# Kernel optimization log

Measured on AMD Instinct MI355X. Metric: run time of the kernel, lower is better.

## Reference

```python
import jax, jax.numpy as jnp
import numpy as np

N_HEAD = 16
MASKED_BIAS = -10000.0


def setup_inputs() -> dict:
    key = jax.random.key(0)
    k1, k2, k3 = jax.random.split(key, 3)
    B, S, D = 2, 2048, 1024
    scale_in = 0.02  # GPT-2 style init scale for weights
    return {
        "hidden_states": jax.random.normal(k1, (B, S, D), dtype=jnp.float32),
        "c_attn_w": jax.random.normal(k2, (D, 3 * D), dtype=jnp.float32) * scale_in,
        "c_attn_b": jnp.zeros((3 * D,), dtype=jnp.float32),
        "c_proj_w": jax.random.normal(k3, (D, D), dtype=jnp.float32) * scale_in,
        "c_proj_b": jnp.zeros((D,), dtype=jnp.float32),
    }


def reference(hidden_states, c_attn_w, c_attn_b, c_proj_w, c_proj_b):
    B, S, D = hidden_states.shape
    H = N_HEAD
    hd = D // H

    # Conv1D (HF): x @ W + b, fused QKV
    qkv = hidden_states @ c_attn_w + c_attn_b          # [B, S, 3D]
    q, k, v = jnp.split(qkv, 3, axis=-1)

    def to_heads(x):  # [B, S, D] -> [B, H, S, hd]
        return x.reshape(B, S, H, hd).transpose(0, 2, 1, 3)

    q, k, v = to_heads(q), to_heads(k), to_heads(v)

    # scaled scores (scale=True divides by sqrt(head_dim))
    w = jnp.einsum("bhqd,bhkd->bhqk", q, k) / jnp.float32(hd) ** 0.5  # [B,H,S,S]

    # causal mask via torch.where(mask, w, masked_bias)
    causal = jnp.tril(jnp.ones((S, S), dtype=bool))
    w = jnp.where(causal, w, jnp.float32(MASKED_BIAS))

    w = jax.nn.softmax(w, axis=-1)
    # attn_dropout / resid_dropout are identity in eval mode

    out = jnp.einsum("bhqk,bhkd->bhqd", w, v)          # [B,H,S,hd]
    out = out.transpose(0, 2, 1, 3).reshape(B, S, D)   # merge heads

    return out @ c_proj_w + c_proj_b                   # [B,S,D]
```

## Files before the change

kernel.cpp:

```cpp
#include <hip/hip_runtime.h>
#include <hip/hip_bf16.h>

typedef __attribute__((ext_vector_type(8))) short bf16x8;
typedef __attribute__((ext_vector_type(4))) float f32x4;
typedef __attribute__((ext_vector_type(4))) unsigned u32x4;

#define B_SZ 2
#define S_SZ 2048
#define D_SZ 1024
#define H_SZ 16
#define HD_SZ 64

static __device__ __forceinline__ short f2bf(float f) {
    unsigned u = __builtin_bit_cast(unsigned, f);
    u += 0x7FFFu + ((u >> 16) & 1u);
    return (short)(u >> 16);
}

static __device__ __forceinline__ float fexp2(float x) {
    float r; asm("v_exp_f32 %0, %1" : "=v"(r) : "v"(x)); return r;
}

static __device__ __forceinline__ unsigned cvtpk(float lo, float hi) {
    unsigned r; asm("v_cvt_pk_bf16_f32 %0, %1, %2" : "=v"(r) : "v"(lo), "v"(hi)); return r;
}

static __device__ __forceinline__ void gload16(const short* g, short* l) {
    __builtin_amdgcn_global_load_lds(
        (const __attribute__((address_space(1))) unsigned*)g,
        (__attribute__((address_space(3))) unsigned*)l,
        16, 0, 0);
}

#define SBAR() do { __builtin_amdgcn_sched_barrier(0); \
                    __builtin_amdgcn_s_barrier(); \
                    __builtin_amdgcn_sched_barrier(0); } while (0)

__global__ __launch_bounds__(256) void k_prep(const float* __restrict__ hs, short* __restrict__ Xb,
                                              const float* __restrict__ w1, short* __restrict__ W1T,
                                              const float* __restrict__ w2, short* __restrict__ W2T) {
    __shared__ float tile[32][33];
    const int id = blockIdx.x;
    const int tid = threadIdx.x;
    if (id < 4096) {
        int i = (id * 256 + tid) * 4;
        float4 v = *reinterpret_cast<const float4*>(hs + i);
        short4 o;
        o.x = f2bf(v.x); o.y = f2bf(v.y); o.z = f2bf(v.z); o.w = f2bf(v.w);
        *reinterpret_cast<short4*>(Xb + i) = o;
        return;
    }
    const float* in;
    short* out;
    int N, bx, by;
    if (id < 7168) {
        int bid = id - 4096;
        in = w1; out = W1T; N = 3072;
        bx = bid % 96; by = bid / 96;
    } else {
        int bid = id - 7168;
        in = w2; out = W2T; N = 1024;
        bx = bid & 31; by = bid >> 5;
    }
    const int k0 = by * 32, n0 = bx * 32;
    const int tx = tid & 31, ty = tid >> 5;
    #pragma unroll
    for (int i = 0; i < 4; ++i)
        tile[ty + i * 8][tx] = in[(size_t)(k0 + ty + i * 8) * N + n0 + tx];
    __syncthreads();
    #pragma unroll
    for (int i = 0; i < 4; ++i)
        out[(size_t)(n0 + ty + i * 8) * 1024 + k0 + tx] = f2bf(tile[tx][ty + i * 8]);
}

__global__ __launch_bounds__(512, 1) void k_gemm_qkv8(
    const short* __restrict__ A, const short* __restrict__ Bt,
    const float* __restrict__ bias,
    short* __restrict__ Qo, short* __restrict__ Ko, short* __restrict__ VTo) {
    constexpr int K = 1024, NT = 16;
    __shared__ short As[2][256 * 64];
    __shared__ short Bs[2][192 * 64];
    const int tid = threadIdx.x;
    const int lane = tid & 63;
    const int w = tid >> 6;
    const int wr = w >> 2, wc = w & 3;
    const int lr = lane & 15, lc = lane >> 4;
    const int bid = blockIdx.x;
    const int xcd = bid & 7, local = bid >> 3;
    const int bm = (xcd >> 1) * 4 + (local >> 3);
    const int bn = (xcd & 1) * 8 + (local & 7);
    const size_t arow0 = (size_t)bm * 256;
    const size_t brow0 = (size_t)bn * 192;

    const int srl = tid >> 3;
    const int sc8 = (tid & 7) ^ (srl & 7);
    const int dcol = (tid & 7) * 8;

    f32x4 acc[8][3];
    #pragma unroll
    for (int m = 0; m < 8; ++m)
        #pragma unroll
        for (int n = 0; n < 3; ++n)
            acc[m][n] = (f32x4){0.f, 0.f, 0.f, 0.f};

    auto STAGE_A = [&](int T) {
        const int buf = T & 1;
        #pragma unroll
        for (int j = 0; j < 4; ++j) {
            int row = j * 64 + srl;
            gload16(&A[(arow0 + row) * K + T * 64 + sc8 * 8], &As[buf][row * 64 + dcol]);
        }
    };
    auto STAGE_B = [&](int T) {
        const int buf = T & 1;
        #pragma unroll
        for (int j = 0; j < 3; ++j) {
            int row = j * 64 + srl;
            gload16(&Bt[(brow0 + row) * K + T * 64 + sc8 * 8], &Bs[buf][row * 64 + dcol]);
        }
    };

    const int rx = (lr & 7) * 8;
    auto LDA = [&](int buf, int rowoff, int c) {
        return *reinterpret_cast<const bf16x8*>(
            &As[buf][(wr * 128 + rowoff + lr) * 64 + (((c * 32) + lc * 8) ^ rx)]);
    };
    auto LDB = [&](int buf, int n, int c) {
        return *reinterpret_cast<const bf16x8*>(
            &Bs[buf][(wc * 48 + n * 16 + lr) * 64 + (((c * 32) + lc * 8) ^ rx)]);
    };

    bf16x8 at[4][2];
    bf16x8 bfr[3][2];

    STAGE_A(0); STAGE_B(0); STAGE_B(1);
    asm volatile("s_waitcnt vmcnt(3)" ::: "memory");
    SBAR();

    for (int T = 0; T < NT; ++T) {
        const int buf = T & 1;
        #pragma unroll
        for (int m = 0; m < 4; ++m)
            #pragma unroll
            for (int c = 0; c < 2; ++c)
                at[m][c] = LDA(buf, m * 16, c);
        #pragma unroll
        for (int n = 0; n < 3; ++n)
            #pragma unroll
            for (int c = 0; c < 2; ++c)
                bfr[n][c] = LDB(buf, n, c);
        if (T + 1 < NT) STAGE_A(T + 1);
        SBAR();
        __builtin_amdgcn_s_setprio(1);
        #pragma unroll
        for (int m = 0; m < 4; ++m)
            #pragma unroll
            for (int n = 0; n < 3; ++n)
                #pragma unroll
                for (int c = 0; c < 2; ++c)
                    acc[m][n] = __builtin_amdgcn_mfma_f32_16x16x32_bf16(at[m][c], bfr[n][c], acc[m][n], 0, 0, 0);
        __builtin_amdgcn_s_setprio(0);
        SBAR();
        #pragma unroll
        for (int m = 0; m < 4; ++m)
            #pragma unroll
            for (int c = 0; c < 2; ++c)
                at[m][c] = LDA(buf, 64 + m * 16, c);
        if (T + 2 < NT) {
            STAGE_B(T + 2);
            asm volatile("s_waitcnt vmcnt(3)" ::: "memory");
        } else {
            asm volatile("s_waitcnt vmcnt(0)" ::: "memory");
        }
        SBAR();
        __builtin_amdgcn_s_setprio(1);
        #pragma unroll
        for (int m = 0; m < 4; ++m)
            #pragma unroll
            for (int n = 0; n < 3; ++n)
                #pragma unroll
                for (int c = 0; c < 2; ++c)
                    acc[4 + m][n] = __builtin_amdgcn_mfma_f32_16x16x32_bf16(at[m][c], bfr[n][c], acc[4 + m][n], 0, 0, 0);
        __builtin_amdgcn_s_setprio(0);
        SBAR();
    }

    #pragma unroll
    for (int n = 0; n < 3; ++n) {
        const int col = bn * 192 + wc * 48 + n * 16 + lr;
        const float bv = bias[col];
        if (col < 2048) {
            const bool isq = (col < 1024);
            const float scale = isq ? 0.18033688011112042f : 1.0f;
            short* dst = isq ? Qo : Ko;
            const int dg = col & 1023;
            const int hh = dg >> 6, dd = dg & 63;
            #pragma unroll
            for (int m = 0; m < 8; ++m) {
                #pragma unroll
                for (int r = 0; r < 4; ++r) {
                    int grow = bm * 256 + wr * 128 + m * 16 + lc * 4 + r;
                    int b = grow >> 11, s = grow & 2047;
                    dst[(((size_t)(b * H_SZ + hh)) * S_SZ + s) * HD_SZ + dd] = f2bf((acc[m][n][r] + bv) * scale);
                }
            }
        } else {
            const int dv = col - 2048;
            const int hh = dv >> 6, dt = dv & 63;
            #pragma unroll
            for (int m = 0; m < 8; ++m) {
                int grow = bm * 256 + wr * 128 + m * 16 + lc * 4;
                int b = grow >> 11, s = grow & 2047;
                short4 st;
                st.x = f2bf(acc[m][n][0] + bv);
                st.y = f2bf(acc[m][n][1] + bv);
                st.z = f2bf(acc[m][n][2] + bv);
                st.w = f2bf(acc[m][n][3] + bv);
                *reinterpret_cast<short4*>(
                    &VTo[(((size_t)(b * H_SZ + hh)) * HD_SZ + dt) * S_SZ + s]) = st;
            }
        }
    }
}

__global__ __launch_bounds__(256) void k_attn(const short* __restrict__ Q,
                                              const short* __restrict__ Kv,
                                              const short* __restrict__ VT,
                                              short* __restrict__ O) {
    __shared__ short Ks[3][64 * 64];
    __shared__ short Vs[3][64 * 64];
    const int id = blockIdx.x;
    const int bh = ((id & 7) << 2) | ((id >> 3) & 3);
    const int h = bh & 15;
    const int bb = bh >> 4;
    const int g = id >> 5, oct = g >> 3, gr = g & 7;
    const int qt = (oct == 0) ? 31 - gr : (oct == 1) ? 16 + gr : (oct == 2) ? 15 - gr : gr;
    const int tid = threadIdx.x;
    const int lane = tid & 63, w = tid >> 6;
    const int lr = lane & 15, lc = lane >> 4;
    const int qrow0 = qt * 64 + w * 16;
    const size_t base = (size_t)bh * S_SZ * HD_SZ;

    bf16x8 qf[2];
    #pragma unroll
    for (int c = 0; c < 2; ++c)
        qf[c] = *reinterpret_cast<const bf16x8*>(&Q[base + (size_t)(qrow0 + lr) * HD_SZ + c * 32 + lc * 8]);

    float l_run = 0.f;
    f32x4 o_acc[4];
    #pragma unroll
    for (int n = 0; n < 4; ++n) o_acc[n] = (f32x4){0.f, 0.f, 0.f, 0.f};

    const int srow = tid >> 3;
    const int sslot = (tid & 7) ^ (srow & 7);
    const short* kp = &Kv[base + (size_t)srow * HD_SZ + sslot * 8];
    const short* vp = &VT[base + (size_t)srow * S_SZ + sslot * 8];
    auto STAGE = [&](int b) {
        gload16(kp, &Ks[b][tid * 8]);
        gload16(kp + 2048, &Ks[b][2048 + tid * 8]);
        gload16(vp, &Vs[b][tid * 8]);
        gload16(vp + 32 * S_SZ, &Vs[b][2048 + tid * 8]);
        kp += 4096; vp += 64;
    };

    const int q_row = qrow0 + lr;
    const int rxa = (lr & 7) * 8;
    const bool b0 = (lane & 16) != 0;
    const bool b1 = (lane & 32) != 0;

    STAGE(0);
    if (qt >= 1) {
        STAGE(1);
        asm volatile("s_waitcnt vmcnt(4)" ::: "memory");
    } else {
        asm volatile("s_waitcnt vmcnt(0)" ::: "memory");
    }
    SBAR();

    int bufc = 0, stc = 2;
    for (int kt = 0; kt <= qt; ++kt) {
        if (kt + 2 <= qt) STAGE(stc);
        {
            f32x4 sf[4];
            __builtin_amdgcn_s_setprio(1);
            #pragma unroll
            for (int n = 0; n < 4; ++n) {
                f32x4 z = (f32x4){0.f, 0.f, 0.f, 0.f};
                #pragma unroll
                for (int c = 0; c < 2; ++c) {
                    bf16x8 kf = *reinterpret_cast<const bf16x8*>(
                        &Ks[bufc][(n * 16 + lr) * 64 + ((c * 32 + lc * 8) ^ rxa)]);
                    z = __builtin_amdgcn_mfma_f32_16x16x32_bf16(kf, qf[c], z, 0, 0, 0);
                }
                sf[n] = z;
            }
            __builtin_amdgcn_s_setprio(0);
            if (kt == qt) {
                const int kb = kt * 64 + lc * 4 - q_row;
                #pragma unroll
                for (int n = 0; n < 4; ++n)
                    #pragma unroll
                    for (int r = 0; r < 4; ++r)
                        sf[n][r] = (kb + n * 16 + r > 0) ? -14427.0f : sf[n][r];
            }
            float rs = 0.f;
            #pragma unroll
            for (int n = 0; n < 4; ++n)
                #pragma unroll
                for (int r = 0; r < 4; ++r) {
                    float pv = fexp2(sf[n][r]);
                    sf[n][r] = pv;
                    rs += pv;
                }
            l_run += rs;
            unsigned Apk0 = cvtpk(sf[0][0], sf[0][1]), Apk1 = cvtpk(sf[0][2], sf[0][3]);
            unsigned Bpk0 = cvtpk(sf[1][0], sf[1][1]), Bpk1 = cvtpk(sf[1][2], sf[1][3]);
            unsigned Cpk0 = cvtpk(sf[2][0], sf[2][1]), Cpk1 = cvtpk(sf[2][2], sf[2][3]);
            unsigned Dpk0 = cvtpk(sf[3][0], sf[3][1]), Dpk1 = cvtpk(sf[3][2], sf[3][3]);
            unsigned x0 = __shfl_xor(b0 ? Apk0 : Bpk0, 16);
            unsigned x1 = __shfl_xor(b0 ? Apk1 : Bpk1, 16);
            unsigned x2 = __shfl_xor(b0 ? Cpk0 : Dpk0, 16);
            unsigned x3 = __shfl_xor(b0 ? Cpk1 : Dpk1, 16);
            unsigned y0 = __shfl_xor(b1 ? Apk0 : Bpk0, 32);
            unsigned y1 = __shfl_xor(b1 ? Apk1 : Bpk1, 32);
            unsigned y2 = __shfl_xor(b1 ? Cpk0 : Dpk0, 32);
            unsigned y3 = __shfl_xor(b1 ? Cpk1 : Dpk1, 32);
            unsigned z0 = __shfl_xor(b1 ? Apk0 : Bpk0, 48);
            unsigned z1 = __shfl_xor(b1 ? Apk1 : Bpk1, 48);
            unsigned z2 = __shfl_xor(b1 ? Cpk0 : Dpk0, 48);
            unsigned z3 = __shfl_xor(b1 ? Cpk1 : Dpk1, 48);
            u32x4 pv0 = { b1 ? (b0 ? x0 : y0) : (b0 ? z0 : Apk0),
                          b1 ? (b0 ? x1 : y1) : (b0 ? z1 : Apk1),
                          b1 ? (b0 ? Bpk0 : z0) : (b0 ? y0 : x0),
                          b1 ? (b0 ? Bpk1 : z1) : (b0 ? y1 : x1) };
            u32x4 pv1 = { b1 ? (b0 ? x2 : y2) : (b0 ? z2 : Cpk0),
                          b1 ? (b0 ? x3 : y3) : (b0 ? z3 : Cpk1),
                          b1 ? (b0 ? Dpk0 : z2) : (b0 ? y2 : x2),
                          b1 ? (b0 ? Dpk1 : z3) : (b0 ? y3 : x3) };
            bf16x8 paA = __builtin_bit_cast(bf16x8, pv0);
            bf16x8 paB = __builtin_bit_cast(bf16x8, pv1);
            __builtin_amdgcn_s_setprio(1);
            #pragma unroll
            for (int c = 0; c < 2; ++c) {
                bf16x8 pa = c ? paB : paA;
                #pragma unroll
                for (int n = 0; n < 4; ++n) {
                    bf16x8 vf = *reinterpret_cast<const bf16x8*>(
                        &Vs[bufc][(n * 16 + lr) * 64 + ((c * 32 + lc * 8) ^ rxa)]);
                    o_acc[n] = __builtin_amdgcn_mfma_f32_16x16x32_bf16(pa, vf, o_acc[n], 0, 0, 0);
                }
            }
            __builtin_amdgcn_s_setprio(0);
        }
        if (kt < qt) {
            if (kt + 2 <= qt) asm volatile("s_waitcnt vmcnt(4)" ::: "memory");
            else              asm volatile("s_waitcnt vmcnt(0)" ::: "memory");
            SBAR();
        }
        bufc = (bufc == 2) ? 0 : bufc + 1;
        stc  = (stc == 2) ? 0 : stc + 1;
    }

    l_run += __shfl_xor(l_run, 16);
    l_run += __shfl_xor(l_run, 32);
    float li[4];
    #pragma unroll
    for (int r = 0; r < 4; ++r)
        li[r] = 1.0f / __shfl(l_run, lc * 4 + r);
    #pragma unroll
    for (int n = 0; n < 4; ++n) {
        #pragma unroll
        for (int r = 0; r < 4; ++r) {
            float v = o_acc[n][r] * li[r];
            int s = qrow0 + lc * 4 + r;
            O[((size_t)bb * S_SZ + s) * D_SZ + h * 64 + n * 16 + lr] = f2bf(v);
        }
    }
}

__global__ __launch_bounds__(256, 2) void k_gemm_proj(
    const short* __restrict__ A, const short* __restrict__ Bt,
    const float* __restrict__ bias, float* __restrict__ out) {
    constexpr int K = 1024, NT = 16, N = 1024;
    __shared__ short As[2][128 * 64];
    __shared__ short Bs[2][128 * 64];
    const int tid = threadIdx.x;
    const int lane = tid & 63;
    const int w = tid >> 6;
    const int wr = w >> 1, wc = w & 1;
    const int lr = lane & 15, lc = lane >> 4;
    const int bid = blockIdx.x;
    const int xcd = bid & 7, local = bid >> 3;
    const int bm = xcd * 4 + (local & 3);
    const int bn = local >> 2;
    const size_t arow0 = (size_t)bm * 128;
    const size_t brow0 = (size_t)bn * 128;

    const int srl = tid >> 3;
    const int sc8 = (tid & 7) ^ (srl & 7);
    const int dcol = (tid & 7) * 8;

    f32x4 acc[4][4];
    #pragma unroll
    for (int m = 0; m < 4; ++m)
        #pragma unroll
        for (int n = 0; n < 4; ++n)
            acc[m][n] = (f32x4){0.f, 0.f, 0.f, 0.f};

    auto STAGE_A = [&](int T) {
        const int buf = T & 1;
        #pragma unroll
        for (int j = 0; j < 4; ++j) {
            int row = j * 32 + srl;
            gload16(&A[(arow0 + row) * K + T * 64 + sc8 * 8], &As[buf][row * 64 + dcol]);
        }
    };
    auto STAGE_B = [&](int T) {
        const int buf = T & 1;
        #pragma unroll
        for (int j = 0; j < 4; ++j) {
            int row = j * 32 + srl;
            gload16(&Bt[(brow0 + row) * K + T * 64 + sc8 * 8], &Bs[buf][row * 64 + dcol]);
        }
    };

    const int rx = (lr & 7) * 8;
    auto LDA = [&](int buf, int rowoff, int c) {
        return *reinterpret_cast<const bf16x8*>(
            &As[buf][(wr * 64 + rowoff + lr) * 64 + (((c * 32) + lc * 8) ^ rx)]);
    };
    auto LDB = [&](int buf, int n, int c) {
        return *reinterpret_cast<const bf16x8*>(
            &Bs[buf][(wc * 64 + n * 16 + lr) * 64 + (((c * 32) + lc * 8) ^ rx)]);
    };

    bf16x8 at[2][2];
    bf16x8 bfr[4][2];

    STAGE_A(0); STAGE_B(0); STAGE_B(1);
    asm volatile("s_waitcnt vmcnt(4)" ::: "memory");
    SBAR();

    for (int T = 0; T < NT; ++T) {
        const int buf = T & 1;
        #pragma unroll
        for (int m = 0; m < 2; ++m)
            #pragma unroll
            for (int c = 0; c < 2; ++c)
                at[m][c] = LDA(buf, m * 16, c);
        #pragma unroll
        for (int n = 0; n < 4; ++n)
            #pragma unroll
            for (int c = 0; c < 2; ++c)
                bfr[n][c] = LDB(buf, n, c);
        if (T + 1 < NT) STAGE_A(T + 1);
        SBAR();
        __builtin_amdgcn_s_setprio(1);
        #pragma unroll
        for (int m = 0; m < 2; ++m)
            #pragma unroll
            for (int n = 0; n < 4; ++n)
                #pragma unroll
                for (int c = 0; c < 2; ++c)
                    acc[m][n] = __builtin_amdgcn_mfma_f32_16x16x32_bf16(at[m][c], bfr[n][c], acc[m][n], 0, 0, 0);
        __builtin_amdgcn_s_setprio(0);
        SBAR();
        #pragma unroll
        for (int m = 0; m < 2; ++m)
            #pragma unroll
            for (int c = 0; c < 2; ++c)
                at[m][c] = LDA(buf, 32 + m * 16, c);
        if (T + 2 < NT) {
            STAGE_B(T + 2);
            asm volatile("s_waitcnt vmcnt(4)" ::: "memory");
        } else {
            asm volatile("s_waitcnt vmcnt(0)" ::: "memory");
        }
        SBAR();
        __builtin_amdgcn_s_setprio(1);
        #pragma unroll
        for (int m = 0; m < 2; ++m)
            #pragma unroll
            for (int n = 0; n < 4; ++n)
                #pragma unroll
                for (int c = 0; c < 2; ++c)
                    acc[2 + m][n] = __builtin_amdgcn_mfma_f32_16x16x32_bf16(at[m][c], bfr[n][c], acc[2 + m][n], 0, 0, 0);
        __builtin_amdgcn_s_setprio(0);
        SBAR();
    }

    #pragma unroll
    for (int n = 0; n < 4; ++n) {
        const int col = bn * 128 + wc * 64 + n * 16 + lr;
        const float bv = bias[col];
        #pragma unroll
        for (int m = 0; m < 4; ++m) {
            #pragma unroll
            for (int r = 0; r < 4; ++r) {
                int grow = bm * 128 + wr * 64 + m * 16 + lc * 4 + r;
                out[(size_t)grow * N + col] = acc[m][n][r] + bv;
            }
        }
    }
}

extern "C" void kernel_launch(void* const* d_in, const int* in_sizes, int n_in,
                              void* d_out, int out_size, void* d_ws, size_t ws_size,
                              hipStream_t stream) {
    (void)in_sizes; (void)n_in; (void)out_size; (void)ws_size;
    const float* hs     = (const float*)d_in[0];
    const float* w_attn = (const float*)d_in[1];
    const float* b_attn = (const float*)d_in[2];
    const float* w_proj = (const float*)d_in[3];
    const float* b_proj = (const float*)d_in[4];
    float* out = (float*)d_out;
    char* ws = (char*)d_ws;

    short* Xb  = (short*)(ws + 0);
    short* W1T = (short*)(ws + 8388608);
    short* W2T = (short*)(ws + 14680064);
    short* Qb  = (short*)(ws + 16777216);
    short* Kb  = (short*)(ws + 25165824);
    short* VTb = (short*)(ws + 33554432);
    short* Ob  = (short*)(ws + 0);

    k_prep<<<dim3(8192), dim3(256), 0, stream>>>(hs, Xb, w_attn, W1T, w_proj, W2T);
    k_gemm_qkv8<<<dim3(256), dim3(512), 0, stream>>>(Xb, W1T, b_attn, Qb, Kb, VTb);
    k_attn<<<dim3(1024), dim3(256), 0, stream>>>(Qb, Kb, VTb, Ob);
    k_gemm_proj<<<dim3(256), dim3(256), 0, stream>>>(Ob, W2T, b_proj, out);
}
```

Before: 98.12 us.

## Software-pipeline QK^T of next tile with softmax and PV of current tile

```diff
diff --git a/kernel.cpp b/kernel.cpp
--- a/kernel.cpp
+++ b/kernel.cpp
@@ -227,8 +227,8 @@
                                               const short* __restrict__ Kv,
                                               const short* __restrict__ VT,
                                               short* __restrict__ O) {
-    __shared__ short Ks[3][64 * 64];
-    __shared__ short Vs[3][64 * 64];
+    __shared__ short Ks[4][64 * 64];
+    __shared__ short Vs[4][64 * 64];
     const int id = blockIdx.x;
     const int bh = ((id & 7) << 2) | ((id >> 3) & 3);
     const int h = bh & 15;
@@ -268,6 +268,22 @@
     const bool b0 = (lane & 16) != 0;
     const bool b1 = (lane & 32) != 0;
 
+    auto QK = [&](f32x4* s, int b) {
+        __builtin_amdgcn_s_setprio(1);
+        #pragma unroll
+        for (int n = 0; n < 4; ++n) {
+            f32x4 z = (f32x4){0.f, 0.f, 0.f, 0.f};
+            #pragma unroll
+            for (int c = 0; c < 2; ++c) {
+                bf16x8 kf = *reinterpret_cast<const bf16x8*>(
+                    &Ks[b][(n * 16 + lr) * 64 + ((c * 32 + lc * 8) ^ rxa)]);
+                z = __builtin_amdgcn_mfma_f32_16x16x32_bf16(kf, qf[c], z, 0, 0, 0);
+            }
+            s[n] = z;
+        }
+        __builtin_amdgcn_s_setprio(0);
+    };
+
     STAGE(0);
     if (qt >= 1) {
         STAGE(1);
@@ -276,89 +292,78 @@
         asm volatile("s_waitcnt vmcnt(0)" ::: "memory");
     }
     SBAR();
-
-    int bufc = 0, stc = 2;
-    for (int kt = 0; kt <= qt; ++kt) {
-        if (kt + 2 <= qt) STAGE(stc);
-        {
-            f32x4 sf[4];
-            __builtin_amdgcn_s_setprio(1);
-            #pragma unroll
-            for (int n = 0; n < 4; ++n) {
-                f32x4 z = (f32x4){0.f, 0.f, 0.f, 0.f};
-                #pragma unroll
-                for (int c = 0; c < 2; ++c) {
-                    bf16x8 kf = *reinterpret_cast<const bf16x8*>(
-                        &Ks[bufc][(n * 16 + lr) * 64 + ((c * 32 + lc * 8) ^ rxa)]);
-                    z = __builtin_amdgcn_mfma_f32_16x16x32_bf16(kf, qf[c], z, 0, 0, 0);
-                }
-                sf[n] = z;
-            }
-            __builtin_amdgcn_s_setprio(0);
-            if (kt == qt) {
-                const int kb = kt * 64 + lc * 4 - q_row;
-                #pragma unroll
-                for (int n = 0; n < 4; ++n)
-                    #pragma unroll
-                    for (int r = 0; r < 4; ++r)
-                        sf[n][r] = (kb + n * 16 + r > 0) ? -14427.0f : sf[n][r];
-            }
-            float rs = 0.f;
+    f32x4 sf[4];
+    QK(sf, 0);
+
+    for (int i = 0; i <= qt; ++i) {
+        const int bcur = i & 3, bnext = (i + 1) & 3, bst = (i + 2) & 3;
+        if (i + 2 <= qt) {
+            STAGE(bst);
+            asm volatile("s_waitcnt vmcnt(4)" ::: "memory");
+        } else {
+            asm volatile("s_waitcnt vmcnt(0)" ::: "memory");
+        }
+        SBAR();
+        f32x4 sfn[4];
+        if (i < qt) QK(sfn, bnext);
+        if (i == qt) {
+            const int kb = i * 64 + lc * 4 - q_row;
             #pragma unroll
             for (int n = 0; n < 4; ++n)
                 #pragma unroll
-                for (int r = 0; r < 4; ++r) {
-                    float pv = fexp2(sf[n][r]);
-                    sf[n][r] = pv;
-                    rs += pv;
-                }
-            l_run += rs;
-            unsigned Apk0 = cvtpk(sf[0][0], sf[0][1]), Apk1 = cvtpk(sf[0][2], sf[0][3]);
-            unsigned Bpk0 = cvtpk(sf[1][0], sf[1][1]), Bpk1 = cvtpk(sf[1][2], sf[1][3]);
-            unsigned Cpk0 = cvtpk(sf[2][0], sf[2][1]), Cpk1 = cvtpk(sf[2][2], sf[2][3]);
-            unsigned Dpk0 = cvtpk(sf[3][0], sf[3][1]), Dpk1 = cvtpk(sf[3][2], sf[3][3]);
-            unsigned x0 = __shfl_xor(b0 ? Apk0 : Bpk0, 16);
-            unsigned x1 = __shfl_xor(b0 ? Apk1 : Bpk1, 16);
-            unsigned x2 = __shfl_xor(b0 ? Cpk0 : Dpk0, 16);
-            unsigned x3 = __shfl_xor(b0 ? Cpk1 : Dpk1, 16);
-            unsigned y0 = __shfl_xor(b1 ? Apk0 : Bpk0, 32);
-            unsigned y1 = __shfl_xor(b1 ? Apk1 : Bpk1, 32);
-            unsigned y2 = __shfl_xor(b1 ? Cpk0 : Dpk0, 32);
-            unsigned y3 = __shfl_xor(b1 ? Cpk1 : Dpk1, 32);
-            unsigned z0 = __shfl_xor(b1 ? Apk0 : Bpk0, 48);
-            unsigned z1 = __shfl_xor(b1 ? Apk1 : Bpk1, 48);
-            unsigned z2 = __shfl_xor(b1 ? Cpk0 : Dpk0, 48);
-            unsigned z3 = __shfl_xor(b1 ? Cpk1 : Dpk1, 48);
-            u32x4 pv0 = { b1 ? (b0 ? x0 : y0) : (b0 ? z0 : Apk0),
-                          b1 ? (b0 ? x1 : y1) : (b0 ? z1 : Apk1),
-                          b1 ? (b0 ? Bpk0 : z0) : (b0 ? y0 : x0),
-                          b1 ? (b0 ? Bpk1 : z1) : (b0 ? y1 : x1) };
-            u32x4 pv1 = { b1 ? (b0 ? x2 : y2) : (b0 ? z2 : Cpk0),
-                          b1 ? (b0 ? x3 : y3) : (b0 ? z3 : Cpk1),
-                          b1 ? (b0 ? Dpk0 : z2) : (b0 ? y2 : x2),
-                          b1 ? (b0 ? Dpk1 : z3) : (b0 ? y3 : x3) };
-            bf16x8 paA = __builtin_bit_cast(bf16x8, pv0);
-            bf16x8 paB = __builtin_bit_cast(bf16x8, pv1);
-            __builtin_amdgcn_s_setprio(1);
-            #pragma unroll
-            for (int c = 0; c < 2; ++c) {
-                bf16x8 pa = c ? paB : paA;
-                #pragma unroll
-                for (int n = 0; n < 4; ++n) {
-                    bf16x8 vf = *reinterpret_cast<const bf16x8*>(
-                        &Vs[bufc][(n * 16 + lr) * 64 + ((c * 32 + lc * 8) ^ rxa)]);
-                    o_acc[n] = __builtin_amdgcn_mfma_f32_16x16x32_bf16(pa, vf, o_acc[n], 0, 0, 0);
-                }
+                for (int r = 0; r < 4; ++r)
+                    sf[n][r] = (kb + n * 16 + r > 0) ? -14427.0f : sf[n][r];
+        }
+        float rs = 0.f;
+        #pragma unroll
+        for (int n = 0; n < 4; ++n)
+            #pragma unroll
+            for (int r = 0; r < 4; ++r) {
+                float pv = fexp2(sf[n][r]);
+                sf[n][r] = pv;
+                rs += pv;
             }
-            __builtin_amdgcn_s_setprio(0);
-        }
-        if (kt < qt) {
-            if (kt + 2 <= qt) asm volatile("s_waitcnt vmcnt(4)" ::: "memory");
-            else              asm volatile("s_waitcnt vmcnt(0)" ::: "memory");
-            SBAR();
-        }
-        bufc = (bufc == 2) ? 0 : bufc + 1;
-        stc  = (stc == 2) ? 0 : stc + 1;
+        l_run += rs;
+        unsigned Apk0 = cvtpk(sf[0][0], sf[0][1]), Apk1 = cvtpk(sf[0][2], sf[0][3]);
+        unsigned Bpk0 = cvtpk(sf[1][0], sf[1][1]), Bpk1 = cvtpk(sf[1][2], sf[1][3]);
+        unsigned Cpk0 = cvtpk(sf[2][0], sf[2][1]), Cpk1 = cvtpk(sf[2][2], sf[2][3]);
+        unsigned Dpk0 = cvtpk(sf[3][0], sf[3][1]), Dpk1 = cvtpk(sf[3][2], sf[3][3]);
+        unsigned x0 = __shfl_xor(b0 ? Apk0 : Bpk0, 16);
+        unsigned x1 = __shfl_xor(b0 ? Apk1 : Bpk1, 16);
+        unsigned x2 = __shfl_xor(b0 ? Cpk0 : Dpk0, 16);
+        unsigned x3 = __shfl_xor(b0 ? Cpk1 : Dpk1, 16);
+        unsigned y0 = __shfl_xor(b1 ? Apk0 : Bpk0, 32);
+        unsigned y1 = __shfl_xor(b1 ? Apk1 : Bpk1, 32);
+        unsigned y2 = __shfl_xor(b1 ? Cpk0 : Dpk0, 32);
+        unsigned y3 = __shfl_xor(b1 ? Cpk1 : Dpk1, 32);
+        unsigned z0 = __shfl_xor(b1 ? Apk0 : Bpk0, 48);
+        unsigned z1 = __shfl_xor(b1 ? Apk1 : Bpk1, 48);
+        unsigned z2 = __shfl_xor(b1 ? Cpk0 : Dpk0, 48);
+        unsigned z3 = __shfl_xor(b1 ? Cpk1 : Dpk1, 48);
+        u32x4 pv0 = { b1 ? (b0 ? x0 : y0) : (b0 ? z0 : Apk0),
+                      b1 ? (b0 ? x1 : y1) : (b0 ? z1 : Apk1),
+                      b1 ? (b0 ? Bpk0 : z0) : (b0 ? y0 : x0),
+                      b1 ? (b0 ? Bpk1 : z1) : (b0 ? y1 : x1) };
+        u32x4 pv1 = { b1 ? (b0 ? x2 : y2) : (b0 ? z2 : Cpk0),
+                      b1 ? (b0 ? x3 : y3) : (b0 ? z3 : Cpk1),
+                      b1 ? (b0 ? Dpk0 : z2) : (b0 ? y2 : x2),
+                      b1 ? (b0 ? Dpk1 : z3) : (b0 ? y3 : x3) };
+        bf16x8 paA = __builtin_bit_cast(bf16x8, pv0);
+        bf16x8 paB = __builtin_bit_cast(bf16x8, pv1);
+        __builtin_amdgcn_s_setprio(1);
+        #pragma unroll
+        for (int c = 0; c < 2; ++c) {
+            bf16x8 pa = c ? paB : paA;
+            #pragma unroll
+            for (int n = 0; n < 4; ++n) {
+                bf16x8 vf = *reinterpret_cast<const bf16x8*>(
+                    &Vs[bcur][(n * 16 + lr) * 64 + ((c * 32 + lc * 8) ^ rxa)]);
+                o_acc[n] = __builtin_amdgcn_mfma_f32_16x16x32_bf16(pa, vf, o_acc[n], 0, 0, 0);
+            }
+        }
+        __builtin_amdgcn_s_setprio(0);
+        #pragma unroll
+        for (int n = 0; n < 4; ++n) sf[n] = sfn[n];
     }
 
     l_run += __shfl_xor(l_run, 16);
```

Measured after the change: 101.1 us. 3.1% more time.
